# Kernel tuning notes

Measured on AMD Instinct MI355X. Metric: run time of the kernel, lower is better.

## Reference

```python
import jax, jax.numpy as jnp
import numpy as np

def setup_inputs() -> dict:
    key = jax.random.key(0)
    ks = jax.random.split(key, 8)
    b, n, dim = 2, 2048, 512
    h, d, K, M = 8, 64, 32, 131072
    x = jax.random.normal(ks[0], (b, n, dim), dtype=jnp.float32)
    mem_db = jax.random.normal(ks[1], (b, M, 2, d), dtype=jnp.float32)
    knn_idx = jax.random.randint(ks[2], (b, h, n, K), 0, M)
    mem_mask = jax.random.randint(ks[3], (b, h, n, K), 0, 2).astype(bool)
    Wq = jax.random.normal(ks[4], (h * d, dim), dtype=jnp.float32) * 0.02
    Wkv = jax.random.normal(ks[5], (2 * d, dim), dtype=jnp.float32) * 0.02
    Wout = jax.random.normal(ks[6], (dim, h * d), dtype=jnp.float32) * 0.02
    scale_param = jnp.ones((h, 1, 1), dtype=jnp.float32) * np.log(20.0)
    return {"x": x, "mem_db": mem_db, "knn_idx": knn_idx, "mem_mask": mem_mask,
            "Wq": Wq, "Wkv": Wkv, "Wout": Wout, "scale_param": scale_param}

def reference(x, mem_db, knn_idx, mem_mask, Wq, Wkv, Wout, scale_param):
    b, n, dim = x.shape
    h = scale_param.shape[0]
    d = Wq.shape[0] // h
    # projections
    q = jnp.einsum('bnc,ec->bne', x, Wq).reshape(b, n, h, d).transpose(0, 2, 1, 3)  # b h n d
    q = q / jnp.linalg.norm(q, axis=-1, keepdims=True).clip(1e-12)  # l2norm
    kv = jnp.einsum('bnc,ec->bne', x, Wkv)  # [b,n,2d]; detached + added to memory (side effect only)
    scale = jnp.exp(scale_param)  # [h,1,1]
    # per-query KNN gather: mem_db [b,M,2,d], knn_idx [b,h,n,K] -> [b,h,n,K,2,d]
    mem_kv = jax.vmap(lambda db, ix: db[ix])(mem_db, knn_idx)
    mem_k = mem_kv[..., 0, :]  # b h n K d
    mem_v = mem_kv[..., 1, :]
    sim = jnp.einsum('bhid,bhijd->bhij', q, mem_k) * scale  # b h n K
    mask_value = -jnp.finfo(sim.dtype).max
    sim = jnp.where(mem_mask, sim, mask_value)
    attn = jax.nn.softmax(sim, axis=-1)  # stable softmax
    out = jnp.einsum('bhij,bhijd->bhid', attn, mem_v)  # b h n d
    out = out.transpose(0, 2, 1, 3).reshape(b, n, h * d)
    return jnp.einsum('bne,ce->bnc', out, Wout)
```

## Files before the change

### kernel.cpp

```cpp
#include <hip/hip_runtime.h>
#include <hip/hip_bf16.h>
#include <math.h>

#define B_SZ 2
#define N_SEQ 2048
#define DIM 512
#define H_HEADS 8
#define D_HEAD 64
#define K_NN 32
#define M_DB 131072

typedef __attribute__((ext_vector_type(8))) short bf16x8;
typedef __attribute__((ext_vector_type(4))) float f32x4;

__device__ __forceinline__ void cvt_hi_lo(float f, short& h, short& l) {
    unsigned u = __float_as_uint(f);
    unsigned uh = u + (0x7fffu + ((u >> 16) & 1u));
    h = (short)(uh >> 16);
    float r = f - __uint_as_float((uh >> 16) << 16);
    unsigned ur = __float_as_uint(r);
    l = (short)((ur + (0x7fffu + ((ur >> 16) & 1u))) >> 16);
}

__device__ __forceinline__ void split4(float4 a, ushort4& h, ushort4& l) {
    short hh, ll;
    cvt_hi_lo(a.x, hh, ll); h.x = hh; l.x = ll;
    cvt_hi_lo(a.y, hh, ll); h.y = hh; l.y = ll;
    cvt_hi_lo(a.z, hh, ll); h.z = hh; l.z = ll;
    cvt_hi_lo(a.w, hh, ll); h.w = hh; l.w = ll;
}

__global__ __launch_bounds__(256) void prep_kernel(
    const float4* __restrict__ x, const float4* __restrict__ wq,
    const float4* __restrict__ wout,
    ushort4* __restrict__ xhi, ushort4* __restrict__ xlo,
    ushort4* __restrict__ qhi, ushort4* __restrict__ qlo,
    ushort4* __restrict__ ohi, ushort4* __restrict__ olo,
    const unsigned char* __restrict__ mb, int* __restrict__ flag)
{
    const int bid = blockIdx.x;
    const int t = threadIdx.x;
    if (bid < 2048) {
        int i = bid * 256 + t;
        ushort4 h, l;
        split4(x[i], h, l);
        xhi[i] = h; xlo[i] = l;
    } else if (bid < 2560) {
        int i = (bid - 2048) * 256 + t;
        const int n4 = DIM * DIM / 4;
        const float4* src = (i < n4) ? wq : wout;
        ushort4* dh = (i < n4) ? qhi : ohi;
        ushort4* dl = (i < n4) ? qlo : olo;
        int j = (i < n4) ? i : i - n4;
        ushort4 h, l;
        split4(src[j], h, l);
        dh[j] = h; dl[j] = l;
    } else {
        if (t < 64) {
            unsigned char v = 0;
            for (int e = t; e < 1024; e += 64) {
                v |= mb[4 * e + 1];
                v |= mb[4 * e + 2];
                v |= mb[4 * e + 3];
            }
            unsigned long long any = __ballot(v != 0);
            if (t == 0) *flag = (any != 0ull) ? 1 : 0;
        }
    }
}

__global__ __launch_bounds__(256) void gemm_mfma_planes(
    const unsigned short* __restrict__ Ahi, const unsigned short* __restrict__ Alo,
    const unsigned short* __restrict__ Bhi, const unsigned short* __restrict__ Blo,
    float* __restrict__ C, int Mdim, int Ndim, int Kdim)
{
    const int t = threadIdx.x;
    const int wave = t >> 6, lane = t & 63;
    const int r = lane & 15, qd = lane >> 4;
    const int m0 = blockIdx.x * 64 + (wave & 1) * 32;
    const int n0 = blockIdx.y * 64 + (wave >> 1) * 32;

    f32x4 acc[2][2];
#pragma unroll
    for (int i = 0; i < 2; ++i)
#pragma unroll
        for (int j = 0; j < 2; ++j) acc[i][j] = (f32x4){0.f, 0.f, 0.f, 0.f};

    const size_t a0 = (size_t)(m0 + r) * Kdim + qd * 8;
    const size_t a1 = a0 + (size_t)16 * Kdim;
    const size_t b0 = (size_t)(n0 + r) * Kdim + qd * 8;
    const size_t b1 = b0 + (size_t)16 * Kdim;

    for (int k0 = 0; k0 < Kdim; k0 += 32) {
        bf16x8 ah0 = *(const bf16x8*)(Ahi + a0 + k0);
        bf16x8 ah1 = *(const bf16x8*)(Ahi + a1 + k0);
        bf16x8 al0 = *(const bf16x8*)(Alo + a0 + k0);
        bf16x8 al1 = *(const bf16x8*)(Alo + a1 + k0);
        bf16x8 bh0 = *(const bf16x8*)(Bhi + b0 + k0);
        bf16x8 bh1 = *(const bf16x8*)(Bhi + b1 + k0);
        bf16x8 bl0 = *(const bf16x8*)(Blo + b0 + k0);
        bf16x8 bl1 = *(const bf16x8*)(Blo + b1 + k0);

        acc[0][0] = __builtin_amdgcn_mfma_f32_16x16x32_bf16(ah0, bh0, acc[0][0], 0, 0, 0);
        acc[0][1] = __builtin_amdgcn_mfma_f32_16x16x32_bf16(ah0, bh1, acc[0][1], 0, 0, 0);
        acc[1][0] = __builtin_amdgcn_mfma_f32_16x16x32_bf16(ah1, bh0, acc[1][0], 0, 0, 0);
        acc[1][1] = __builtin_amdgcn_mfma_f32_16x16x32_bf16(ah1, bh1, acc[1][1], 0, 0, 0);

        acc[0][0] = __builtin_amdgcn_mfma_f32_16x16x32_bf16(ah0, bl0, acc[0][0], 0, 0, 0);
        acc[0][1] = __builtin_amdgcn_mfma_f32_16x16x32_bf16(ah0, bl1, acc[0][1], 0, 0, 0);
        acc[1][0] = __builtin_amdgcn_mfma_f32_16x16x32_bf16(ah1, bl0, acc[1][0], 0, 0, 0);
        acc[1][1] = __builtin_amdgcn_mfma_f32_16x16x32_bf16(ah1, bl1, acc[1][1], 0, 0, 0);

        acc[0][0] = __builtin_amdgcn_mfma_f32_16x16x32_bf16(al0, bh0, acc[0][0], 0, 0, 0);
        acc[0][1] = __builtin_amdgcn_mfma_f32_16x16x32_bf16(al0, bh1, acc[0][1], 0, 0, 0);
        acc[1][0] = __builtin_amdgcn_mfma_f32_16x16x32_bf16(al1, bh0, acc[1][0], 0, 0, 0);
        acc[1][1] = __builtin_amdgcn_mfma_f32_16x16x32_bf16(al1, bh1, acc[1][1], 0, 0, 0);
    }

#pragma unroll
    for (int mt = 0; mt < 2; ++mt)
#pragma unroll
        for (int nt = 0; nt < 2; ++nt)
#pragma unroll
            for (int rr = 0; rr < 4; ++rr)
                C[(size_t)(m0 + mt * 16 + qd * 4 + rr) * Ndim + n0 + nt * 16 + r] =
                    acc[mt][nt][rr];
}

__global__ __launch_bounds__(256) void attn_kernel(
    const float* __restrict__ qbuf,
    const float* __restrict__ mem_db,
    const int* __restrict__ knn_idx,
    const void* __restrict__ mem_mask,
    const float* __restrict__ scale_param,
    const int* __restrict__ flag,
    unsigned short* __restrict__ out_hi,
    unsigned short* __restrict__ out_lo)
{
    const int wave = blockIdx.x * 4 + (threadIdx.x >> 6);
    const int lane = threadIdx.x & 63;
    const int sub = lane & 15, grp = lane >> 4;
    const int i = wave % N_SEQ;
    const int bh = wave / N_SEQ;
    const int hi = bh % H_HEADS;
    const int bi = bh / H_HEADS;

    const int bytelayout = *flag;

    const float* qrow = qbuf + (size_t)(bi * N_SEQ + i) * DIM + hi * D_HEAD;
    float qv = qrow[lane];
    float ss = qv * qv;
#pragma unroll
    for (int s = 32; s; s >>= 1) ss += __shfl_xor(ss, s);
    qv = qv / fmaxf(sqrtf(ss), 1e-12f);

    float q4[4];
#pragma unroll
    for (int c = 0; c < 4; ++c) q4[c] = __shfl(qv, 4 * sub + c);

    const float scale = __expf(scale_param[hi]);

    const size_t kb = ((size_t)(bi * H_HEADS + hi) * N_SEQ + i) * K_NN;
    int idxv = 0, maskv = 0;
    if (lane < K_NN) {
        idxv = knn_idx[kb + lane];
        if (bytelayout)
            maskv = ((const unsigned char*)mem_mask)[kb + lane] ? 1 : 0;
        else
            maskv = ((const int*)mem_mask)[kb + lane] ? 1 : 0;
    }

    unsigned long long mbits = __ballot(maskv != 0);
    const bool allmasked = (mbits == 0ull);

    const float* dbb = mem_db + (size_t)bi * M_DB * (2 * D_HEAD);

    float4 kk[8], vv[8];
#pragma unroll
    for (int g = 0; g < 8; ++g) {
        int idx = __shfl(idxv, 4 * g + grp);
        bool mrow = (mbits >> (4 * g + grp)) & 1ull;
        size_t koff = mrow ? (size_t)idx * (2 * D_HEAD) : 0;
        size_t voff = (mrow || allmasked) ? (size_t)idx * (2 * D_HEAD) : 0;
        kk[g] = *(const float4*)(dbb + koff + 4 * sub);
        vv[g] = *(const float4*)(dbb + voff + D_HEAD + 4 * sub);
    }

    float s8[8];
#pragma unroll
    for (int g = 0; g < 8; ++g) {
        float p = q4[0] * kk[g].x + q4[1] * kk[g].y + q4[2] * kk[g].z + q4[3] * kk[g].w;
        p += __shfl_xor(p, 1);
        p += __shfl_xor(p, 2);
        p += __shfl_xor(p, 4);
        p += __shfl_xor(p, 8);
        s8[g] = p;
    }

    float simlane = -INFINITY;
#pragma unroll
    for (int g = 0; g < 8; ++g) {
        float tv = __shfl(s8[g], (lane & 3) << 4);
        if ((lane >> 2) == g) simlane = tv;
    }
    if (lane < K_NN)
        simlane = maskv ? simlane * scale : -3.402823466e38f;

    float m = simlane;
#pragma unroll
    for (int s = 32; s; s >>= 1) m = fmaxf(m, __shfl_xor(m, s));
    float w = __expf(simlane - m);
    float l = w;
#pragma unroll
    for (int s = 32; s; s >>= 1) l += __shfl_xor(l, s);
    float winv = w / l;

    float4 o = {0.f, 0.f, 0.f, 0.f};
#pragma unroll
    for (int g = 0; g < 8; ++g) {
        float wg = __shfl(winv, 4 * g + grp);
        o.x = fmaf(wg, vv[g].x, o.x);
        o.y = fmaf(wg, vv[g].y, o.y);
        o.z = fmaf(wg, vv[g].z, o.z);
        o.w = fmaf(wg, vv[g].w, o.w);
    }
#pragma unroll
    for (int s = 16; s <= 32; s <<= 1) {
        o.x += __shfl_xor(o.x, s);
        o.y += __shfl_xor(o.y, s);
        o.z += __shfl_xor(o.z, s);
        o.w += __shfl_xor(o.w, s);
    }
    if (grp == 0) {
        ushort4 h, l4;
        split4(o, h, l4);
        size_t off = ((size_t)(bi * N_SEQ + i) * DIM + hi * D_HEAD + 4 * sub) >> 2;
        ((ushort4*)out_hi)[off] = h;
        ((ushort4*)out_lo)[off] = l4;
    }
}

extern "C" void kernel_launch(void* const* d_in, const int* in_sizes, int n_in,
                              void* d_out, int out_size, void* d_ws, size_t ws_size,
                              hipStream_t stream) {
    const float* x        = (const float*)d_in[0];
    const float* mem_db   = (const float*)d_in[1];
    const int*   knn_idx  = (const int*)d_in[2];
    const void*  mem_mask = d_in[3];
    const float* Wq       = (const float*)d_in[4];
    const float* Wout     = (const float*)d_in[6];
    const float* scale_p  = (const float*)d_in[7];
    float* out = (float*)d_out;

    const int Mrows = B_SZ * N_SEQ;
    const int n_x   = Mrows * DIM;
    const int n_w   = DIM * DIM;

    char* ws = (char*)d_ws;
    int* flag = (int*)ws;
    float* qbuf = (float*)(ws + 256);
    unsigned short* x_hi  = (unsigned short*)(qbuf + (size_t)n_x);
    unsigned short* x_lo  = x_hi + n_x;
    unsigned short* ao_hi = x_lo + n_x;
    unsigned short* ao_lo = ao_hi + n_x;
    unsigned short* wq_hi = ao_lo + n_x;
    unsigned short* wq_lo = wq_hi + n_w;
    unsigned short* wo_hi = wq_lo + n_w;
    unsigned short* wo_lo = wo_hi + n_w;

    prep_kernel<<<2561, 256, 0, stream>>>(
        (const float4*)x, (const float4*)Wq, (const float4*)Wout,
        (ushort4*)x_hi, (ushort4*)x_lo,
        (ushort4*)wq_hi, (ushort4*)wq_lo, (ushort4*)wo_hi, (ushort4*)wo_lo,
        (const unsigned char*)mem_mask, flag);

    dim3 ggrid(Mrows / 64, DIM / 64);
    gemm_mfma_planes<<<ggrid, 256, 0, stream>>>(x_hi, x_lo, wq_hi, wq_lo, qbuf,
                                                Mrows, DIM, DIM);

    const int n_waves = B_SZ * H_HEADS * N_SEQ;
    attn_kernel<<<n_waves / 4, 256, 0, stream>>>(qbuf, mem_db, knn_idx, mem_mask,
                                                 scale_p, flag, ao_hi, ao_lo);

    gemm_mfma_planes<<<ggrid, 256, 0, stream>>>(ao_hi, ao_lo, wo_hi, wo_lo, out,
                                                Mrows, DIM, DIM);
}
```

Before: 288.3 us.

## Stage GEMM operand tiles through double-buffered LDS with direct global-to-LDS loads

Rewrites the split-bf16 projection GEMM so each block cooperatively loads 64-wide K slices of the hi/lo A and B planes into LDS using global_load_lds. The loads go into two buffers, so the next slice is fetched while MFMAs run on the current one. This removes redundant global reads of the same operand rows by different waves and hides load latency. It costs 64KB of LDS per block, which may limit occupancy, and adds a barrier each K step.

```diff
diff --git a/kernel.cpp b/kernel.cpp
--- a/kernel.cpp
+++ b/kernel.cpp
@@ -12,6 +12,11 @@
 
 typedef __attribute__((ext_vector_type(8))) short bf16x8;
 typedef __attribute__((ext_vector_type(4))) float f32x4;
+
+#define GLL16(g, l)                                                       \
+    __builtin_amdgcn_global_load_lds(                                     \
+        (const __attribute__((address_space(1))) unsigned int*)(g),       \
+        (__attribute__((address_space(3))) unsigned int*)(l), 16, 0, 0)
 
 __device__ __forceinline__ void cvt_hi_lo(float f, short& h, short& l) {
     unsigned u = __float_as_uint(f);
@@ -69,16 +74,32 @@
     }
 }
 
-__global__ __launch_bounds__(256) void gemm_mfma_planes(
+__global__ __launch_bounds__(256) void gemm_mfma_lds(
     const unsigned short* __restrict__ Ahi, const unsigned short* __restrict__ Alo,
     const unsigned short* __restrict__ Bhi, const unsigned short* __restrict__ Blo,
     float* __restrict__ C, int Mdim, int Ndim, int Kdim)
 {
+    __shared__ char lds[2][32768];
     const int t = threadIdx.x;
-    const int wave = t >> 6, lane = t & 63;
+    const int w = t >> 6, lane = t & 63;
     const int r = lane & 15, qd = lane >> 4;
-    const int m0 = blockIdx.x * 64 + (wave & 1) * 32;
-    const int n0 = blockIdx.y * 64 + (wave >> 1) * 32;
+    const int wm = w & 1, wn = w >> 1;
+    const int m0 = blockIdx.x * 64;
+    const int n0 = blockIdx.y * 64;
+
+    const unsigned short* gsrc[8];
+#pragma unroll
+    for (int j = 0; j < 8; ++j) {
+        const int cl = j * 4 + w;
+        const int isB = cl >> 4;
+        const int c = cl & 15;
+        const int p = c >> 3, s = (c >> 2) & 1, h = c & 3;
+        const int row = (isB ? n0 : m0) + 16 * h + r;
+        const int col = 32 * s + 8 * qd;
+        const unsigned short* plane =
+            isB ? (p ? Blo : Bhi) : (p ? Alo : Ahi);
+        gsrc[j] = plane + (size_t)row * Kdim + col;
+    }
 
     f32x4 acc[2][2];
 #pragma unroll
@@ -86,45 +107,64 @@
 #pragma unroll
         for (int j = 0; j < 2; ++j) acc[i][j] = (f32x4){0.f, 0.f, 0.f, 0.f};
 
-    const size_t a0 = (size_t)(m0 + r) * Kdim + qd * 8;
-    const size_t a1 = a0 + (size_t)16 * Kdim;
-    const size_t b0 = (size_t)(n0 + r) * Kdim + qd * 8;
-    const size_t b1 = b0 + (size_t)16 * Kdim;
-
-    for (int k0 = 0; k0 < Kdim; k0 += 32) {
-        bf16x8 ah0 = *(const bf16x8*)(Ahi + a0 + k0);
-        bf16x8 ah1 = *(const bf16x8*)(Ahi + a1 + k0);
-        bf16x8 al0 = *(const bf16x8*)(Alo + a0 + k0);
-        bf16x8 al1 = *(const bf16x8*)(Alo + a1 + k0);
-        bf16x8 bh0 = *(const bf16x8*)(Bhi + b0 + k0);
-        bf16x8 bh1 = *(const bf16x8*)(Bhi + b1 + k0);
-        bf16x8 bl0 = *(const bf16x8*)(Blo + b0 + k0);
-        bf16x8 bl1 = *(const bf16x8*)(Blo + b1 + k0);
-
-        acc[0][0] = __builtin_amdgcn_mfma_f32_16x16x32_bf16(ah0, bh0, acc[0][0], 0, 0, 0);
-        acc[0][1] = __builtin_amdgcn_mfma_f32_16x16x32_bf16(ah0, bh1, acc[0][1], 0, 0, 0);
-        acc[1][0] = __builtin_amdgcn_mfma_f32_16x16x32_bf16(ah1, bh0, acc[1][0], 0, 0, 0);
-        acc[1][1] = __builtin_amdgcn_mfma_f32_16x16x32_bf16(ah1, bh1, acc[1][1], 0, 0, 0);
-
-        acc[0][0] = __builtin_amdgcn_mfma_f32_16x16x32_bf16(ah0, bl0, acc[0][0], 0, 0, 0);
-        acc[0][1] = __builtin_amdgcn_mfma_f32_16x16x32_bf16(ah0, bl1, acc[0][1], 0, 0, 0);
-        acc[1][0] = __builtin_amdgcn_mfma_f32_16x16x32_bf16(ah1, bl0, acc[1][0], 0, 0, 0);
-        acc[1][1] = __builtin_amdgcn_mfma_f32_16x16x32_bf16(ah1, bl1, acc[1][1], 0, 0, 0);
-
-        acc[0][0] = __builtin_amdgcn_mfma_f32_16x16x32_bf16(al0, bh0, acc[0][0], 0, 0, 0);
-        acc[0][1] = __builtin_amdgcn_mfma_f32_16x16x32_bf16(al0, bh1, acc[0][1], 0, 0, 0);
-        acc[1][0] = __builtin_amdgcn_mfma_f32_16x16x32_bf16(al1, bh0, acc[1][0], 0, 0, 0);
-        acc[1][1] = __builtin_amdgcn_mfma_f32_16x16x32_bf16(al1, bh1, acc[1][1], 0, 0, 0);
-    }
-
-#pragma unroll
-    for (int mt = 0; mt < 2; ++mt)
-#pragma unroll
-        for (int nt = 0; nt < 2; ++nt)
+    auto stage = [&](int buf, int kstep) {
+#pragma unroll
+        for (int j = 0; j < 8; ++j) {
+            const int cl = j * 4 + w;
+            GLL16(gsrc[j] + kstep * 64, &lds[buf][cl * 1024]);
+        }
+    };
+
+    auto compute = [&](int buf) {
+        const char* base = lds[buf];
+        bf16x8 A8[2][2][2], B8[2][2][2];
+#pragma unroll
+        for (int p = 0; p < 2; ++p)
+#pragma unroll
+            for (int s = 0; s < 2; ++s)
+#pragma unroll
+                for (int i = 0; i < 2; ++i) {
+                    A8[p][s][i] = *(const bf16x8*)(
+                        base + ((p * 2 + s) * 4 + 2 * wm + i) * 1024 + lane * 16);
+                    B8[p][s][i] = *(const bf16x8*)(
+                        base + 16384 +
+                        ((p * 2 + s) * 4 + 2 * wn + i) * 1024 + lane * 16);
+                }
+#pragma unroll
+        for (int s = 0; s < 2; ++s)
+#pragma unroll
+            for (int mi = 0; mi < 2; ++mi)
+#pragma unroll
+                for (int ni = 0; ni < 2; ++ni) {
+                    acc[mi][ni] = __builtin_amdgcn_mfma_f32_16x16x32_bf16(
+                        A8[0][s][mi], B8[0][s][ni], acc[mi][ni], 0, 0, 0);
+                    acc[mi][ni] = __builtin_amdgcn_mfma_f32_16x16x32_bf16(
+                        A8[0][s][mi], B8[1][s][ni], acc[mi][ni], 0, 0, 0);
+                    acc[mi][ni] = __builtin_amdgcn_mfma_f32_16x16x32_bf16(
+                        A8[1][s][mi], B8[0][s][ni], acc[mi][ni], 0, 0, 0);
+                }
+    };
+
+    const int nsteps = Kdim >> 6;
+    stage(0, 0);
+    asm volatile("s_waitcnt vmcnt(0)" ::: "memory");
+    __syncthreads();
+    for (int ks = 0; ks < nsteps - 1; ++ks) {
+        stage((ks + 1) & 1, ks + 1);
+        compute(ks & 1);
+        asm volatile("s_waitcnt vmcnt(0)" ::: "memory");
+        __syncthreads();
+    }
+    compute((nsteps - 1) & 1);
+
+#pragma unroll
+    for (int mi = 0; mi < 2; ++mi)
+#pragma unroll
+        for (int ni = 0; ni < 2; ++ni)
 #pragma unroll
             for (int rr = 0; rr < 4; ++rr)
-                C[(size_t)(m0 + mt * 16 + qd * 4 + rr) * Ndim + n0 + nt * 16 + r] =
-                    acc[mt][nt][rr];
+                C[(size_t)(m0 + 32 * wm + 16 * mi + qd * 4 + rr) * Ndim +
+                  n0 + 32 * wn + 16 * ni + r] = acc[mi][ni][rr];
 }
 
 __global__ __launch_bounds__(256) void attn_kernel(
@@ -275,13 +315,13 @@
         (const unsigned char*)mem_mask, flag);
 
     dim3 ggrid(Mrows / 64, DIM / 64);
-    gemm_mfma_planes<<<ggrid, 256, 0, stream>>>(x_hi, x_lo, wq_hi, wq_lo, qbuf,
-                                                Mrows, DIM, DIM);
+    gemm_mfma_lds<<<ggrid, 256, 0, stream>>>(x_hi, x_lo, wq_hi, wq_lo, qbuf,
+                                             Mrows, DIM, DIM);
 
     const int n_waves = B_SZ * H_HEADS * N_SEQ;
     attn_kernel<<<n_waves / 4, 256, 0, stream>>>(qbuf, mem_db, knn_idx, mem_mask,
                                                  scale_p, flag, ao_hi, ao_lo);
 
-    gemm_mfma_planes<<<ggrid, 256, 0, stream>>>(ao_hi, ao_lo, wo_hi, wo_lo, out,
-                                                Mrows, DIM, DIM);
-}
+    gemm_mfma_lds<<<ggrid, 256, 0, stream>>>(ao_hi, ao_lo, wo_hi, wo_lo, out,
+                                             Mrows, DIM, DIM);
+}
```

Result: faster. 262.9 us (-8.8%).
